# Kernel tuning notes

Measured on AMD Instinct MI355X. Metric: run time of the kernel, lower is better.

Reference implementation:

```python
import jax, jax.numpy as jnp
import numpy as np

B, S, E = 4, 2048, 1024
H, Dh = 16, 64


def setup_inputs() -> dict:
    key = jax.random.key(0)
    ks = jax.random.split(key, 9)
    scale_in = 1.0 / np.sqrt(E)
    scale_out = 1.0 / np.sqrt(H * Dh)
    x = jax.random.normal(ks[0], (B, S, E), dtype=jnp.float32)
    # Per-head projection weights stacked over heads: [H, E, Dh]
    Wq = jax.random.uniform(ks[1], (H, E, Dh), jnp.float32, -scale_in, scale_in)
    bq = jax.random.uniform(ks[2], (H, Dh), jnp.float32, -scale_in, scale_in)
    Wk = jax.random.uniform(ks[3], (H, E, Dh), jnp.float32, -scale_in, scale_in)
    bk = jax.random.uniform(ks[4], (H, Dh), jnp.float32, -scale_in, scale_in)
    Wv = jax.random.uniform(ks[5], (H, E, Dh), jnp.float32, -scale_in, scale_in)
    bv = jax.random.uniform(ks[6], (H, Dh), jnp.float32, -scale_in, scale_in)
    # Output projection: [H*Dh, E]
    Wo = jax.random.uniform(ks[7], (H * Dh, E), jnp.float32, -scale_out, scale_out)
    bo = jax.random.uniform(ks[8], (E,), jnp.float32, -scale_out, scale_out)
    return {"x": x, "Wq": Wq, "bq": bq, "Wk": Wk, "bk": bk,
            "Wv": Wv, "bv": bv, "Wo": Wo, "bo": bo}


def reference(x, Wq, bq, Wk, bk, Wv, bv, Wo, bo):
    # Per-head linear projections, batched over heads: [B, H, S, Dh]
    q = jnp.einsum('bse,hed->bhsd', x, Wq) + bq[None, :, None, :]
    k = jnp.einsum('bse,hed->bhsd', x, Wk) + bk[None, :, None, :]
    v = jnp.einsum('bse,hed->bhsd', x, Wv) + bv[None, :, None, :]
    scale = 1.0 / jnp.sqrt(jnp.asarray(Dh, dtype=x.dtype))
    scores = jnp.einsum('bhsd,bhtd->bhst', q, k) * scale  # [B, H, S, S]
    weights = jax.nn.softmax(scores, axis=-1)
    z = jnp.einsum('bhst,bhtd->bhsd', weights, v)  # [B, H, S, Dh]
    # Concat heads in module order: [B, S, H*Dh]
    z = jnp.transpose(z, (0, 2, 1, 3)).reshape(B, S, H * Dh)
    return z @ Wo + bo
```

## Files before the change

### kernel.cpp

```cpp
#include <hip/hip_runtime.h>
#include <hip/hip_bf16.h>

#define B_  4
#define S_  2048
#define E_  1024
#define H_  16
#define DH_ 64
#define M_  (B_*S_)
#define HD_ (H_*DH_)

typedef unsigned short u16;
typedef __attribute__((ext_vector_type(8))) __bf16 bf16x8;
typedef __attribute__((ext_vector_type(4))) __bf16 bf16x4;
typedef __attribute__((ext_vector_type(4))) float  f32x4;

#if __has_builtin(__builtin_amdgcn_exp2f)
#define EXP2F __builtin_amdgcn_exp2f
#else
#define EXP2F __builtin_exp2f
#endif

#define QSCALE 0.18033688011112042f

__device__ __forceinline__ void g2l16(const void* g, void* l) {
  __builtin_amdgcn_global_load_lds(
      (const __attribute__((address_space(1))) void*)g,
      (__attribute__((address_space(3))) void*)l, 16, 0, 0);
}

__device__ __forceinline__ u16 f2bf(float f) {
  union { float f; unsigned u; } v; v.f = f;
  unsigned r = v.u + 0x7FFFu + ((v.u >> 16) & 1u);
  return (u16)(r >> 16);
}

__global__ __launch_bounds__(256) void cvt_x_kernel(const float* __restrict__ x,
                                                    u16* __restrict__ xb) {
  int i = blockIdx.x * 256 + threadIdx.x;
  float4 v = ((const float4*)x)[i];
  ushort4 o;
  o.x = f2bf(v.x); o.y = f2bf(v.y); o.z = f2bf(v.z); o.w = f2bf(v.w);
  ((ushort4*)xb)[i] = o;
}

__global__ __launch_bounds__(256) void pack_wqkv_kernel(
    const float* __restrict__ Wq, const float* __restrict__ Wk,
    const float* __restrict__ Wv, u16* __restrict__ wt) {
  __shared__ u16 tile[64][66];
  int p = blockIdx.z, h = blockIdx.y, e0 = blockIdx.x * 64;
  const float* src = (p == 0 ? Wq : (p == 1 ? Wk : Wv)) + h * (E_ * DH_);
  int tid = threadIdx.x;
#pragma unroll
  for (int r = 0; r < 16; ++r) {
    int idx = r * 256 + tid;
    int el = idx >> 6, d = idx & 63;
    tile[el][d] = f2bf(src[(e0 + el) * DH_ + d]);
  }
  __syncthreads();
  u16* dst = wt + (p * HD_ + h * DH_) * E_;
#pragma unroll
  for (int r = 0; r < 16; ++r) {
    int idx = r * 256 + tid;
    int d = idx >> 6, el = idx & 63;
    dst[d * E_ + e0 + el] = tile[el][d];
  }
}

__global__ __launch_bounds__(256) void pack_wo_kernel(const float* __restrict__ Wo,
                                                      u16* __restrict__ wt) {
  __shared__ u16 tile[64][66];
  int c0 = blockIdx.y * 64, e0 = blockIdx.x * 64;
  int tid = threadIdx.x;
#pragma unroll
  for (int r = 0; r < 16; ++r) {
    int idx = r * 256 + tid;
    int cl = idx >> 6, el = idx & 63;
    tile[cl][el] = f2bf(Wo[(c0 + cl) * E_ + e0 + el]);
  }
  __syncthreads();
#pragma unroll
  for (int r = 0; r < 16; ++r) {
    int idx = r * 256 + tid;
    int er = idx >> 6, cl = idx & 63;
    wt[(e0 + er) * HD_ + c0 + cl] = tile[cl][er];
  }
}

__global__ __launch_bounds__(256) void pack_bias_kernel(
    const float* __restrict__ bq, const float* __restrict__ bk,
    const float* __restrict__ bv, float* __restrict__ bb) {
  int i = blockIdx.x * 256 + threadIdx.x;
  const float* s = (i < 1024 ? bq : (i < 2048 ? bk : bv));
  bb[i] = s[i & 1023];
}

template <int MODE>
__global__ __launch_bounds__(256) void gemm_bt_kernel(
    const u16* __restrict__ A, const u16* __restrict__ Bt,
    const float* __restrict__ bias,
    u16* __restrict__ oQ, u16* __restrict__ oK, u16* __restrict__ oV,
    float* __restrict__ oF) {
  constexpr int K = 1024;
  __shared__ __align__(16) u16 As[128 * 32];
  __shared__ __align__(16) u16 Bs[128 * 32];
  const int tid = threadIdx.x;
  const int lane = tid & 63, wv = tid >> 6;
  const int wm = (wv >> 1) * 64, wn = (wv & 1) * 64;
  const int q4 = lane >> 4, lm = lane & 15;
  const int tileM = blockIdx.y * 128, tileN = blockIdx.x * 128;

  const int c0 = tid, c1 = tid + 256;
  const u16* gA0 = A + (tileM + (c0 >> 2)) * K + (((c0 & 3) ^ ((c0 >> 2) & 3)) * 8);
  const u16* gA1 = A + (tileM + (c1 >> 2)) * K + (((c1 & 3) ^ ((c1 >> 2) & 3)) * 8);
  const u16* gB0 = Bt + (tileN + (c0 >> 2)) * K + (((c0 & 3) ^ ((c0 >> 2) & 3)) * 8);
  const u16* gB1 = Bt + (tileN + (c1 >> 2)) * K + (((c1 & 3) ^ ((c1 >> 2) & 3)) * 8);
  u16* lA0 = As + c0 * 8; u16* lA1 = As + c1 * 8;
  u16* lB0 = Bs + c0 * 8; u16* lB1 = Bs + c1 * 8;

  f32x4 acc[4][4] = {};

  int aoff[4], boff[4];
#pragma unroll
  for (int i = 0; i < 4; ++i) {
    int ra = wm + i * 16 + lm;
    aoff[i] = ra * 32 + ((q4 ^ (ra & 3)) * 8);
    int rb = wn + i * 16 + lm;
    boff[i] = rb * 32 + ((q4 ^ (rb & 3)) * 8);
  }

  for (int k0 = 0; k0 < K; k0 += 32) {
    g2l16(gA0 + k0, lA0);
    g2l16(gA1 + k0, lA1);
    g2l16(gB0 + k0, lB0);
    g2l16(gB1 + k0, lB1);
    __syncthreads();
    bf16x8 af[4], bf[4];
#pragma unroll
    for (int i = 0; i < 4; ++i) af[i] = *(const bf16x8*)(As + aoff[i]);
#pragma unroll
    for (int j = 0; j < 4; ++j) bf[j] = *(const bf16x8*)(Bs + boff[j]);
#pragma unroll
    for (int i = 0; i < 4; ++i)
#pragma unroll
      for (int j = 0; j < 4; ++j)
        acc[i][j] = __builtin_amdgcn_mfma_f32_16x16x32_bf16(af[i], bf[j], acc[i][j], 0, 0, 0);
    __syncthreads();
  }

#pragma unroll
  for (int j = 0; j < 4; ++j) {
    int n = tileN + wn + j * 16 + lm;
    float bs = bias[n];
#pragma unroll
    for (int i = 0; i < 4; ++i) {
#pragma unroll
      for (int r = 0; r < 4; ++r) {
        int m = tileM + wm + i * 16 + q4 * 4 + r;
        float val = acc[i][j][r] + bs;
        if (MODE == 1) {
          oF[m * HD_ + n] = val;
        } else {
          int proj = n >> 10, cc = n & 1023;
          if (proj == 0) {
            oQ[m * 1024 + cc] = f2bf(val * QSCALE);
          } else if (proj == 1) {
            oK[m * 1024 + cc] = f2bf(val);
          } else {
            int bb = m >> 11, ss = m & 2047, hh = cc >> 6, dd = cc & 63;
            oV[((bb * H_ + hh) * DH_ + dd) * S_ + ss] = f2bf(val);
          }
        }
      }
    }
  }
}

__global__ __launch_bounds__(256, 3) void flash_kernel(
    const u16* __restrict__ Q, const u16* __restrict__ Kb,
    const u16* __restrict__ Vt, u16* __restrict__ Z) {
  __shared__ __align__(16) u16 Ks[2][64 * 64];
  __shared__ __align__(16) u16 Vs[2][64 * 64];
  __shared__ __align__(16) u16 Ps[4][32 * 64];
  const int tid = threadIdx.x, lane = tid & 63, wv = tid >> 6;
  const int q4 = lane >> 4, lm = lane & 15;

  const int bid = blockIdx.x;
  const int bh = bid >> 4, qt = bid & 15;
  const int b = bh >> 4, h = bh & 15;

  const u16* qbase = Q + ((size_t)(b * S_ + qt * 128)) * HD_ + h * DH_;
  const u16* kbase = Kb + (size_t)b * S_ * HD_ + h * DH_;
  const u16* vbase = Vt + ((size_t)(b * H_ + h)) * DH_ * S_;
  u16* zbase = Z + ((size_t)(b * S_ + qt * 128)) * HD_ + h * DH_;

  const int c0 = tid,       r0 = c0 >> 3, s0 = ((c0 & 7) ^ (r0 & 7)) * 8;
  const int c1 = tid + 256, r1 = c1 >> 3, s1 = ((c1 & 7) ^ (r1 & 7)) * 8;

  bf16x8 qf[2][2];
#pragma unroll
  for (int qs = 0; qs < 2; ++qs)
#pragma unroll
    for (int dc = 0; dc < 2; ++dc)
      qf[qs][dc] = *(const bf16x8*)(qbase + (wv * 32 + qs * 16 + lm) * HD_ + dc * 32 + q4 * 8);

  const bf16x8 ones = {(__bf16)1.f, (__bf16)1.f, (__bf16)1.f, (__bf16)1.f,
                       (__bf16)1.f, (__bf16)1.f, (__bf16)1.f, (__bf16)1.f};

  int koff[4][2], voff[2][4], pwoff[4], proff[2];
#pragma unroll
  for (int kb = 0; kb < 4; ++kb)
#pragma unroll
    for (int dc = 0; dc < 2; ++dc) {
      int row = kb * 16 + lm;
      koff[kb][dc] = row * 64 + (((dc * 4 + q4) ^ (row & 7)) * 8);
    }
#pragma unroll
  for (int ck = 0; ck < 2; ++ck)
#pragma unroll
    for (int db = 0; db < 4; ++db) {
      int row = db * 16 + lm;
      voff[ck][db] = row * 64 + (((ck * 4 + q4) ^ (row & 7)) * 8);
    }
#pragma unroll
  for (int kb = 0; kb < 4; ++kb) {
    int kc = kb * 2 + (q4 >> 1);
    pwoff[kb] = lm * 64 + ((kc ^ (lm & 7)) * 8) + (q4 & 1) * 4;
  }
#pragma unroll
  for (int ck = 0; ck < 2; ++ck)
    proff[ck] = lm * 64 + (((ck * 4 + q4) ^ (lm & 7)) * 8);

  f32x4 oacc[2][4] = {};
  f32x4 liacc[2] = {};
  u16* Pw = Ps[wv];

  {
    g2l16(kbase + r0 * HD_ + s0, Ks[0] + c0 * 8);
    g2l16(kbase + r1 * HD_ + s1, Ks[0] + c1 * 8);
    g2l16(vbase + r0 * S_ + s0, Vs[0] + c0 * 8);
    g2l16(vbase + r1 * S_ + s1, Vs[0] + c1 * 8);
  }

  for (int t = 0; t < 32; ++t) {
    const int pb = t & 1;
    __syncthreads();
    if (t < 31) {
      const u16* kt = kbase + (size_t)(t + 1) * 64 * HD_;
      const u16* vt = vbase + (t + 1) * 64;
      g2l16(kt + r0 * HD_ + s0, Ks[1 - pb] + c0 * 8);
      g2l16(kt + r1 * HD_ + s1, Ks[1 - pb] + c1 * 8);
      g2l16(vt + r0 * S_ + s0, Vs[1 - pb] + c0 * 8);
      g2l16(vt + r1 * S_ + s1, Vs[1 - pb] + c1 * 8);
    }
    const u16* Kp = Ks[pb];
    const u16* Vp = Vs[pb];

#pragma unroll
    for (int kb = 0; kb < 4; ++kb) {
      bf16x8 k0 = *(const bf16x8*)(Kp + koff[kb][0]);
      bf16x8 k1 = *(const bf16x8*)(Kp + koff[kb][1]);
#pragma unroll
      for (int qs = 0; qs < 2; ++qs) {
        f32x4 sc = {};
        sc = __builtin_amdgcn_mfma_f32_16x16x32_bf16(k0, qf[qs][0], sc, 0, 0, 0);
        sc = __builtin_amdgcn_mfma_f32_16x16x32_bf16(k1, qf[qs][1], sc, 0, 0, 0);
        f32x4 p;
#pragma unroll
        for (int r = 0; r < 4; ++r) p[r] = EXP2F(sc[r]);
        bf16x4 pbv = __builtin_convertvector(p, bf16x4);
        *(bf16x4*)(Pw + qs * (16 * 64) + pwoff[kb]) = pbv;
      }
    }
    asm volatile("s_waitcnt lgkmcnt(0)" ::: "memory");

#pragma unroll
    for (int ck = 0; ck < 2; ++ck) {
      bf16x8 pf0 = *(const bf16x8*)(Pw + proff[ck]);
      bf16x8 pf1 = *(const bf16x8*)(Pw + 16 * 64 + proff[ck]);
      liacc[0] = __builtin_amdgcn_mfma_f32_16x16x32_bf16(pf0, ones, liacc[0], 0, 0, 0);
      liacc[1] = __builtin_amdgcn_mfma_f32_16x16x32_bf16(pf1, ones, liacc[1], 0, 0, 0);
#pragma unroll
      for (int db = 0; db < 4; ++db) {
        bf16x8 vf = *(const bf16x8*)(Vp + voff[ck][db]);
        oacc[0][db] = __builtin_amdgcn_mfma_f32_16x16x32_bf16(pf0, vf, oacc[0][db], 0, 0, 0);
        oacc[1][db] = __builtin_amdgcn_mfma_f32_16x16x32_bf16(pf1, vf, oacc[1][db], 0, 0, 0);
      }
    }
  }

#pragma unroll
  for (int qs = 0; qs < 2; ++qs) {
    float rin[4];
#pragma unroll
    for (int r = 0; r < 4; ++r) rin[r] = 1.f / liacc[qs][r];
#pragma unroll
    for (int db = 0; db < 4; ++db)
#pragma unroll
      for (int r = 0; r < 4; ++r)
        zbase[(wv * 32 + qs * 16 + q4 * 4 + r) * HD_ + db * 16 + lm] =
            f2bf(oacc[qs][db][r] * rin[r]);
  }
}

extern "C" void kernel_launch(void* const* d_in, const int* in_sizes, int n_in,
                              void* d_out, int out_size, void* d_ws, size_t ws_size,
                              hipStream_t stream) {
  const float* x  = (const float*)d_in[0];
  const float* Wq = (const float*)d_in[1];
  const float* bq = (const float*)d_in[2];
  const float* Wk = (const float*)d_in[3];
  const float* bk = (const float*)d_in[4];
  const float* Wv = (const float*)d_in[5];
  const float* bv = (const float*)d_in[6];
  const float* Wo = (const float*)d_in[7];
  const float* bo = (const float*)d_in[8];
  float* out = (float*)d_out;

  char* w = (char*)d_ws;
  u16*   xb    = (u16*)w;   w += (size_t)M_ * E_ * 2;
  u16*   wqkvT = (u16*)w;   w += (size_t)3 * HD_ * E_ * 2;
  u16*   woT   = (u16*)w;   w += (size_t)E_ * HD_ * 2;
  float* bqkv  = (float*)w; w += (size_t)3 * HD_ * 4;
  u16*   qB    = (u16*)w;   w += (size_t)M_ * HD_ * 2;
  u16*   kB    = (u16*)w;   w += (size_t)M_ * HD_ * 2;
  u16*   vT    = (u16*)w;   w += (size_t)M_ * HD_ * 2;
  u16*   zB    = (u16*)w;   w += (size_t)M_ * HD_ * 2;

  cvt_x_kernel<<<dim3(M_ * E_ / 4 / 256), 256, 0, stream>>>(x, xb);
  pack_wqkv_kernel<<<dim3(16, 16, 3), 256, 0, stream>>>(Wq, Wk, Wv, wqkvT);
  pack_wo_kernel<<<dim3(16, 16), 256, 0, stream>>>(Wo, woT);
  pack_bias_kernel<<<dim3(12), 256, 0, stream>>>(bq, bk, bv, bqkv);
  gemm_bt_kernel<0><<<dim3(24, 64), 256, 0, stream>>>(xb, wqkvT, bqkv, qB, kB, vT, nullptr);
  flash_kernel<<<dim3(1024), 256, 0, stream>>>(qB, kB, vT, zB);
  gemm_bt_kernel<1><<<dim3(8, 64), 256, 0, stream>>>(zB, woT, bo, nullptr, nullptr, nullptr, out);
}
```

Baseline: 317.1 us.

## Double flash query tile per block and move V transpose to separate kernel

Each flash-attention block now handles 256 query rows (64 per wave) instead of 128, so every K/V tile loaded into LDS is reused across twice as many queries and the grid halves. Occupancy is lowered to 2 blocks per SM and the P buffer doubles. The QKV GEMM now writes V row-major with coalesced stores, and a new LDS-tiled kernel transposes V into the layout the flash kernel expects, replacing the scattered strided stores. The cost is higher register pressure, lower occupancy and an extra kernel launch with its own memory pass.

```diff
diff --git a/kernel.cpp b/kernel.cpp
--- a/kernel.cpp
+++ b/kernel.cpp
@@ -92,6 +92,32 @@
   int i = blockIdx.x * 256 + threadIdx.x;
   const float* s = (i < 1024 ? bq : (i < 2048 ? bk : bv));
   bb[i] = s[i & 1023];
+}
+
+__global__ __launch_bounds__(256) void transpose_v_kernel(
+    const u16* __restrict__ vin, u16* __restrict__ vout) {
+  __shared__ u16 t[64][72];
+  const int tid = threadIdx.x;
+  const int bh = blockIdx.y, st = blockIdx.x * 64;
+  const u16* src = vin + ((size_t)((bh >> 4) * S_ + st)) * HD_ + (bh & 15) * 64;
+#pragma unroll
+  for (int rr = 0; rr < 2; ++rr) {
+    int idx = rr * 256 + tid;
+    int s = idx >> 3, ch = idx & 7;
+    *(uint4*)&t[s][ch * 8] = *(const uint4*)(src + s * HD_ + ch * 8);
+  }
+  __syncthreads();
+  u16* dst = vout + ((size_t)bh) * DH_ * S_ + st;
+#pragma unroll
+  for (int rr = 0; rr < 2; ++rr) {
+    int idx = rr * 256 + tid;
+    int d = idx >> 3, sc = (idx & 7) * 8;
+    ushort4 o0, o1;
+    o0.x = t[sc + 0][d]; o0.y = t[sc + 1][d]; o0.z = t[sc + 2][d]; o0.w = t[sc + 3][d];
+    o1.x = t[sc + 4][d]; o1.y = t[sc + 5][d]; o1.z = t[sc + 6][d]; o1.w = t[sc + 7][d];
+    *(ushort4*)(dst + (size_t)d * S_ + sc) = o0;
+    *(ushort4*)(dst + (size_t)d * S_ + sc + 4) = o1;
+  }
 }
 
 template <int MODE>
@@ -161,47 +187,42 @@
           oF[m * HD_ + n] = val;
         } else {
           int proj = n >> 10, cc = n & 1023;
-          if (proj == 0) {
-            oQ[m * 1024 + cc] = f2bf(val * QSCALE);
-          } else if (proj == 1) {
-            oK[m * 1024 + cc] = f2bf(val);
-          } else {
-            int bb = m >> 11, ss = m & 2047, hh = cc >> 6, dd = cc & 63;
-            oV[((bb * H_ + hh) * DH_ + dd) * S_ + ss] = f2bf(val);
-          }
+          u16* optr = (proj == 0 ? oQ : (proj == 1 ? oK : oV));
+          float scl = (proj == 0 ? QSCALE : 1.0f);
+          optr[m * 1024 + cc] = f2bf(val * scl);
         }
       }
     }
   }
 }
 
-__global__ __launch_bounds__(256, 3) void flash_kernel(
+__global__ __launch_bounds__(256, 2) void flash_kernel(
     const u16* __restrict__ Q, const u16* __restrict__ Kb,
     const u16* __restrict__ Vt, u16* __restrict__ Z) {
   __shared__ __align__(16) u16 Ks[2][64 * 64];
   __shared__ __align__(16) u16 Vs[2][64 * 64];
-  __shared__ __align__(16) u16 Ps[4][32 * 64];
+  __shared__ __align__(16) u16 Ps[4][64 * 64];
   const int tid = threadIdx.x, lane = tid & 63, wv = tid >> 6;
   const int q4 = lane >> 4, lm = lane & 15;
 
   const int bid = blockIdx.x;
-  const int bh = bid >> 4, qt = bid & 15;
+  const int bh = bid >> 3, qt = bid & 7;
   const int b = bh >> 4, h = bh & 15;
 
-  const u16* qbase = Q + ((size_t)(b * S_ + qt * 128)) * HD_ + h * DH_;
+  const u16* qbase = Q + ((size_t)(b * S_ + qt * 256)) * HD_ + h * DH_;
   const u16* kbase = Kb + (size_t)b * S_ * HD_ + h * DH_;
   const u16* vbase = Vt + ((size_t)(b * H_ + h)) * DH_ * S_;
-  u16* zbase = Z + ((size_t)(b * S_ + qt * 128)) * HD_ + h * DH_;
+  u16* zbase = Z + ((size_t)(b * S_ + qt * 256)) * HD_ + h * DH_;
 
   const int c0 = tid,       r0 = c0 >> 3, s0 = ((c0 & 7) ^ (r0 & 7)) * 8;
   const int c1 = tid + 256, r1 = c1 >> 3, s1 = ((c1 & 7) ^ (r1 & 7)) * 8;
 
-  bf16x8 qf[2][2];
-#pragma unroll
-  for (int qs = 0; qs < 2; ++qs)
+  bf16x8 qf[4][2];
+#pragma unroll
+  for (int qs = 0; qs < 4; ++qs)
 #pragma unroll
     for (int dc = 0; dc < 2; ++dc)
-      qf[qs][dc] = *(const bf16x8*)(qbase + (wv * 32 + qs * 16 + lm) * HD_ + dc * 32 + q4 * 8);
+      qf[qs][dc] = *(const bf16x8*)(qbase + (wv * 64 + qs * 16 + lm) * HD_ + dc * 32 + q4 * 8);
 
   const bf16x8 ones = {(__bf16)1.f, (__bf16)1.f, (__bf16)1.f, (__bf16)1.f,
                        (__bf16)1.f, (__bf16)1.f, (__bf16)1.f, (__bf16)1.f};
@@ -230,8 +251,8 @@
   for (int ck = 0; ck < 2; ++ck)
     proff[ck] = lm * 64 + (((ck * 4 + q4) ^ (lm & 7)) * 8);
 
-  f32x4 oacc[2][4] = {};
-  f32x4 liacc[2] = {};
+  f32x4 oacc[4][4] = {};
+  f32x4 liacc[4] = {};
   u16* Pw = Ps[wv];
 
   {
@@ -260,7 +281,7 @@
       bf16x8 k0 = *(const bf16x8*)(Kp + koff[kb][0]);
       bf16x8 k1 = *(const bf16x8*)(Kp + koff[kb][1]);
 #pragma unroll
-      for (int qs = 0; qs < 2; ++qs) {
+      for (int qs = 0; qs < 4; ++qs) {
         f32x4 sc = {};
         sc = __builtin_amdgcn_mfma_f32_16x16x32_bf16(k0, qf[qs][0], sc, 0, 0, 0);
         sc = __builtin_amdgcn_mfma_f32_16x16x32_bf16(k1, qf[qs][1], sc, 0, 0, 0);
@@ -275,21 +296,25 @@
 
 #pragma unroll
     for (int ck = 0; ck < 2; ++ck) {
-      bf16x8 pf0 = *(const bf16x8*)(Pw + proff[ck]);
-      bf16x8 pf1 = *(const bf16x8*)(Pw + 16 * 64 + proff[ck]);
-      liacc[0] = __builtin_amdgcn_mfma_f32_16x16x32_bf16(pf0, ones, liacc[0], 0, 0, 0);
-      liacc[1] = __builtin_amdgcn_mfma_f32_16x16x32_bf16(pf1, ones, liacc[1], 0, 0, 0);
+      bf16x8 pf[4];
+#pragma unroll
+      for (int qs = 0; qs < 4; ++qs)
+        pf[qs] = *(const bf16x8*)(Pw + qs * (16 * 64) + proff[ck]);
+#pragma unroll
+      for (int qs = 0; qs < 4; ++qs)
+        liacc[qs] = __builtin_amdgcn_mfma_f32_16x16x32_bf16(pf[qs], ones, liacc[qs], 0, 0, 0);
 #pragma unroll
       for (int db = 0; db < 4; ++db) {
         bf16x8 vf = *(const bf16x8*)(Vp + voff[ck][db]);
-        oacc[0][db] = __builtin_amdgcn_mfma_f32_16x16x32_bf16(pf0, vf, oacc[0][db], 0, 0, 0);
-        oacc[1][db] = __builtin_amdgcn_mfma_f32_16x16x32_bf16(pf1, vf, oacc[1][db], 0, 0, 0);
+#pragma unroll
+        for (int qs = 0; qs < 4; ++qs)
+          oacc[qs][db] = __builtin_amdgcn_mfma_f32_16x16x32_bf16(pf[qs], vf, oacc[qs][db], 0, 0, 0);
       }
     }
   }
 
 #pragma unroll
-  for (int qs = 0; qs < 2; ++qs) {
+  for (int qs = 0; qs < 4; ++qs) {
     float rin[4];
 #pragma unroll
     for (int r = 0; r < 4; ++r) rin[r] = 1.f / liacc[qs][r];
@@ -297,7 +322,7 @@
     for (int db = 0; db < 4; ++db)
 #pragma unroll
       for (int r = 0; r < 4; ++r)
-        zbase[(wv * 32 + qs * 16 + q4 * 4 + r) * HD_ + db * 16 + lm] =
+        zbase[(wv * 64 + qs * 16 + q4 * 4 + r) * HD_ + db * 16 + lm] =
             f2bf(oacc[qs][db][r] * rin[r]);
   }
 }
@@ -325,12 +350,14 @@
   u16*   kB    = (u16*)w;   w += (size_t)M_ * HD_ * 2;
   u16*   vT    = (u16*)w;   w += (size_t)M_ * HD_ * 2;
   u16*   zB    = (u16*)w;   w += (size_t)M_ * HD_ * 2;
+  u16*   vB    = zB;
 
   cvt_x_kernel<<<dim3(M_ * E_ / 4 / 256), 256, 0, stream>>>(x, xb);
   pack_wqkv_kernel<<<dim3(16, 16, 3), 256, 0, stream>>>(Wq, Wk, Wv, wqkvT);
   pack_wo_kernel<<<dim3(16, 16), 256, 0, stream>>>(Wo, woT);
   pack_bias_kernel<<<dim3(12), 256, 0, stream>>>(bq, bk, bv, bqkv);
-  gemm_bt_kernel<0><<<dim3(24, 64), 256, 0, stream>>>(xb, wqkvT, bqkv, qB, kB, vT, nullptr);
-  flash_kernel<<<dim3(1024), 256, 0, stream>>>(qB, kB, vT, zB);
+  gemm_bt_kernel<0><<<dim3(24, 64), 256, 0, stream>>>(xb, wqkvT, bqkv, qB, kB, vB, nullptr);
+  transpose_v_kernel<<<dim3(32, 64), 256, 0, stream>>>(vB, vT);
+  flash_kernel<<<dim3(512), 256, 0, stream>>>(qB, kB, vT, zB);
   gemm_bt_kernel<1><<<dim3(8, 64), 256, 0, stream>>>(zB, woT, bo, nullptr, nullptr, nullptr, out);
 }
```

New measurement: 290.5 us. -8.4%, faster.
